# Optimization experiments

Hardware: AMD Instinct MI355X
Metric: run time of the kernel (lower is better)

The kernel has to match this reference:

```python
import jax, jax.numpy as jnp
import numpy as np

INPUT_SIZE = 128
HIDDEN_SIZE = 128
B, S = 4, 4096


def setup_inputs() -> dict:
    key = jax.random.key(0)
    ks = jax.random.split(key, 9)
    sc_in = 1.0 / np.sqrt(INPUT_SIZE)
    sc_h = 1.0 / np.sqrt(HIDDEN_SIZE)
    return {
        "x": jax.random.normal(ks[0], (B, S, INPUT_SIZE), jnp.float32),
        "Wq": jax.random.uniform(ks[1], (INPUT_SIZE, HIDDEN_SIZE), jnp.float32, -sc_in, sc_in),
        "bq": jax.random.uniform(ks[2], (HIDDEN_SIZE,), jnp.float32, -sc_in, sc_in),
        "Wk": jax.random.uniform(ks[3], (INPUT_SIZE, HIDDEN_SIZE), jnp.float32, -sc_in, sc_in),
        "bk": jax.random.uniform(ks[4], (HIDDEN_SIZE,), jnp.float32, -sc_in, sc_in),
        "Wv": jax.random.uniform(ks[5], (INPUT_SIZE, HIDDEN_SIZE), jnp.float32, -sc_in, sc_in),
        "bv": jax.random.uniform(ks[6], (HIDDEN_SIZE,), jnp.float32, -sc_in, sc_in),
        "Wo": jax.random.uniform(ks[7], (HIDDEN_SIZE, INPUT_SIZE), jnp.float32, -sc_h, sc_h),
        "bo": jax.random.uniform(ks[8], (INPUT_SIZE,), jnp.float32, -sc_h, sc_h),
    }


def reference(x, Wq, bq, Wk, bk, Wv, bv, Wo, bo):
    # single-head scaled dot-product attention (non-causal), dropout is eval-mode identity
    q = x @ Wq + bq                      # [B, S, H]
    k = x @ Wk + bk                      # [B, S, H]
    v = x @ Wv + bv                      # [B, S, H]
    scale = 1.0 / jnp.sqrt(jnp.asarray(HIDDEN_SIZE, x.dtype))
    scores = jnp.einsum("bsh,bth->bst", q, k) * scale   # [B, S, S]
    attn = jax.nn.softmax(scores, axis=-1)
    attended = jnp.einsum("bst,bth->bsh", attn, v)       # [B, S, H]
    return attended @ Wo + bo                            # [B, S, input_size]
```

## Files before the change

kernel.cpp:

```cpp
#include <hip/hip_runtime.h>
#include <stdint.h>

typedef __attribute__((ext_vector_type(8))) short short8;
typedef __attribute__((ext_vector_type(4))) float f32x4;
typedef __attribute__((ext_vector_type(16))) float f32x16;
typedef __attribute__((ext_vector_type(4))) int i32x4;
typedef __attribute__((ext_vector_type(2))) int i32x2;

#define MFMA16(a, b, c) __builtin_amdgcn_mfma_f32_16x16x32_bf16((a), (b), (c), 0, 0, 0)
#define MFMA32(a, b, c) __builtin_amdgcn_mfma_f32_32x32x16_bf16((a), (b), (c), 0, 0, 0)

typedef __attribute__((address_space(1))) const void GVoid;
typedef __attribute__((address_space(3))) void LVoid;
#define GLDS16(g, l) __builtin_amdgcn_global_load_lds((GVoid*)(g), (LVoid*)(l), 16, 0, 0)

#define L2E 1.4426950408889634f

__device__ __forceinline__ unsigned short f2bf(float f) {
  unsigned int u = __builtin_bit_cast(unsigned int, f);
  u += 0x7fffu + ((u >> 16) & 1u);
  return (unsigned short)(u >> 16);
}
__device__ __forceinline__ float bf2f(unsigned short u) {
  return __builtin_bit_cast(float, (unsigned int)u << 16);
}

__device__ __forceinline__ float fexp2(float x) {
  return __builtin_amdgcn_exp2f(x);
}

__device__ __forceinline__ i32x2 pls(int a, int b) {
  return __builtin_amdgcn_permlane32_swap(a, b, false, false);
}
__device__ __forceinline__ float fasf(int x) { return __builtin_bit_cast(float, x); }
__device__ __forceinline__ int iasi(float x) { return __builtin_bit_cast(int, x); }

__device__ __forceinline__ int cvtpk(float lo, float hi) {
  int d;
  asm("v_cvt_pk_bf16_f32 %0, %1, %2" : "=v"(d) : "v"(lo), "v"(hi));
  return d;
}

__global__ __launch_bounds__(256) void k_proj(
    const float* __restrict__ x,
    const float* __restrict__ Wq, const float* __restrict__ bq,
    const float* __restrict__ Wk, const float* __restrict__ bk,
    const float* __restrict__ Wv, const float* __restrict__ bv,
    const float* __restrict__ Wo,
    unsigned short* __restrict__ Q2, unsigned short* __restrict__ K2,
    unsigned short* __restrict__ V2, unsigned short* __restrict__ Wo2)
{
  __shared__ __align__(16) unsigned short wt[128 * 128];
  __shared__ __align__(16) unsigned short st[64 * 136];
  const int tid  = threadIdx.x;
  const int lane = tid & 63;
  const int wid  = tid >> 6;
  const int l15  = lane & 15;
  const int g    = lane >> 4;
  const int wI   = blockIdx.x >> 8;
  const int blk  = blockIdx.x & 255;
  const int r0   = blk * 64 + wid * 16;

  if (blockIdx.x == 0) {
    for (int e = tid; e < 16384; e += 256) {
      int j = e & 7, ln = (e >> 3) & 63, kt = (e >> 9) & 7, dt = e >> 12;
      int h = kt * 16 + (ln >> 5) * 8 + j, oc = dt * 32 + (ln & 31);
      Wo2[e] = f2bf(Wo[h * 128 + oc]);
    }
  }

  short8 af[4];
  {
    const float* xp = x + (r0 + l15) * 128 + g * 8;
#pragma unroll
    for (int kt = 0; kt < 4; ++kt) {
      float4 v0 = *(const float4*)(xp + kt * 32);
      float4 v1 = *(const float4*)(xp + kt * 32 + 4);
      short8 a;
      a[0] = (short)f2bf(v0.x); a[1] = (short)f2bf(v0.y);
      a[2] = (short)f2bf(v0.z); a[3] = (short)f2bf(v0.w);
      a[4] = (short)f2bf(v1.x); a[5] = (short)f2bf(v1.y);
      a[6] = (short)f2bf(v1.z); a[7] = (short)f2bf(v1.w);
      af[kt] = a;
    }
  }

  const float* W  = (wI == 0) ? Wq : (wI == 1) ? Wk : Wv;
  const float* bv_ = (wI == 0) ? bq : (wI == 1) ? bk : bv;

  for (int i = 0; i < 64; ++i) {
    int idx = i * 256 + tid;
    int k = idx >> 7, n = idx & 127;
    int cs = (k >> 3) ^ (n & 7);
    wt[n * 128 + cs * 8 + (k & 7)] = f2bf(W[idx]);
  }
  __syncthreads();

  float bias[8];
#pragma unroll
  for (int nt = 0; nt < 8; ++nt) bias[nt] = bv_[nt * 16 + l15];

  f32x4 acc[8];
#pragma unroll
  for (int nt = 0; nt < 8; ++nt) acc[nt] = (f32x4){0.f, 0.f, 0.f, 0.f};

#pragma unroll
  for (int nt = 0; nt < 8; ++nt) {
    const int n = nt * 16 + l15;
#pragma unroll
    for (int ks = 0; ks < 4; ++ks) {
      int cs = (ks * 4 + g) ^ (n & 7);
      short8 bf = *(const short8*)&wt[n * 128 + cs * 8];
      acc[nt] = MFMA16(af[ks], bf, acc[nt]);
    }
  }

  if (wI < 2) {
    const float sc = (wI == 0) ? 0.08838834764831845f : 1.0f;
#pragma unroll
    for (int nt = 0; nt < 8; ++nt) {
      int col = nt * 16 + l15;
#pragma unroll
      for (int r = 0; r < 4; ++r)
        st[(wid * 16 + g * 4 + r) * 136 + col] = f2bf((acc[nt][r] + bias[nt]) * sc);
    }
    __syncthreads();
    unsigned short* Og = (wI == 0) ? Q2 : K2;
#pragma unroll
    for (int c4 = 0; c4 < 4; ++c4) {
      int c = c4 * 256 + tid;
      int T = c >> 9, cc = c & 511;
      int kt = cc >> 6, hib = (cc >> 5) & 1, s32 = cc & 31;
      int m0 = blk * 64 + T * 32;
      int bb = m0 >> 12, tile = (m0 & 4095) >> 5;
      short8 v = *(const short8*)&st[(T * 32 + s32) * 136 + kt * 16 + hib * 8];
      *(short8*)&Og[(size_t)(bb * 128 + tile) * 4096 + cc * 8] = v;
    }
  } else {
#pragma unroll
    for (int nt = 0; nt < 8; ++nt) {
      int col = nt * 16 + l15;
      int m0 = r0 + g * 4;
      int bb = m0 >> 12, srow = m0 & 4095;
      int idx = (bb * 128 + (srow >> 5)) * 4096 + ((srow >> 4) & 1) * 2048 +
                (col >> 5) * 512 + ((srow >> 3) & 1) * 256 + (col & 31) * 8 +
                (srow & 7);
      ushort4 pk;
      pk.x = f2bf(acc[nt][0] + bias[nt]);
      pk.y = f2bf(acc[nt][1] + bias[nt]);
      pk.z = f2bf(acc[nt][2] + bias[nt]);
      pk.w = f2bf(acc[nt][3] + bias[nt]);
      *(ushort4*)&V2[idx] = pk;
    }
  }
}

__global__ __launch_bounds__(256, 2) void k_attn(
    const unsigned short* __restrict__ Q2,
    const unsigned short* __restrict__ K2,
    const unsigned short* __restrict__ V2,
    unsigned short* __restrict__ PA,
    float2* __restrict__ ML2)
{
  __shared__ __align__(16) char smem[66560];
  const int tid = threadIdx.x, lane = tid & 63, wid = tid >> 6;
  const int rr = lane & 31, hi = lane >> 5;
  const int p = blockIdx.x;
  const int b = (p & 7) >> 1;
  const int idx = ((p >> 3) << 1) | (p & 1);
  const int qst = idx >> 2, kvq = idx & 3;
  const int q0tile = qst * 4 + wid;

  short8 qf[8];
  {
    const unsigned short* qp = Q2 + (size_t)(b * 128 + q0tile) * 4096 + lane * 8;
#pragma unroll
    for (int kt = 0; kt < 8; ++kt) qf[kt] = *(const short8*)(qp + kt * 512);
  }

  const unsigned short* gsrc[4];
  gsrc[0] = K2 + (size_t)(b * 128 + kvq * 32 + 0) * 4096 + tid * 8;
  gsrc[1] = K2 + (size_t)(b * 128 + kvq * 32 + 1) * 4096 + tid * 8;
  gsrc[2] = V2 + (size_t)(b * 128 + kvq * 32 + 0) * 4096 + tid * 8;
  gsrc[3] = V2 + (size_t)(b * 128 + kvq * 32 + 1) * 4096 + tid * 8;

  char* const rbuf = smem + 65536 + wid * 128;

#pragma unroll
  for (int i = 0; i < 4; ++i) {
    GLDS16(gsrc[i], smem + i * 8192 + tid * 16);
    GLDS16(gsrc[i] + 2048, smem + i * 8192 + 4096 + tid * 16);
  }

  f32x16 O[4];
#pragma unroll
  for (int dt = 0; dt < 4; ++dt)
#pragma unroll
    for (int j = 0; j < 16; ++j) O[dt][j] = 0.f;
  f32x16 zc;
#pragma unroll
  for (int j = 0; j < 16; ++j) zc[j] = 0.f;
  float mS = -3.0e38f, lS = 0.f;

  for (int t = 0; t < 16; ++t) {
    char* const b0 = smem + (t & 1) * 32768;
    if (t < 15) {
      char* const bn = smem + ((t + 1) & 1) * 32768;
      const size_t adv = (size_t)(t + 1) * 8192;
#pragma unroll
      for (int i = 0; i < 4; ++i) {
        GLDS16(gsrc[i] + adv, bn + i * 8192 + tid * 16);
        GLDS16(gsrc[i] + adv + 2048, bn + i * 8192 + 4096 + tid * 16);
      }
      asm volatile("s_waitcnt vmcnt(8)" ::: "memory");
    } else {
      asm volatile("s_waitcnt vmcnt(0)" ::: "memory");
    }
    __builtin_amdgcn_s_barrier();
    __builtin_amdgcn_sched_barrier(0);

    f32x16 sT0, sT1;
    __builtin_amdgcn_s_setprio(1);
    {
      short8 kf[8];
#pragma unroll
      for (int kt = 0; kt < 8; ++kt)
        kf[kt] = *(const short8*)(b0 + kt * 1024 + lane * 16);
      sT0 = MFMA32(kf[0], qf[0], zc);
#pragma unroll
      for (int kt = 1; kt < 8; ++kt) sT0 = MFMA32(kf[kt], qf[kt], sT0);
    }
    {
      short8 kf[8];
#pragma unroll
      for (int kt = 0; kt < 8; ++kt)
        kf[kt] = *(const short8*)(b0 + 8192 + kt * 1024 + lane * 16);
      sT1 = MFMA32(kf[0], qf[0], zc);
#pragma unroll
      for (int kt = 1; kt < 8; ++kt) sT1 = MFMA32(kf[kt], qf[kt], sT1);
    }
    __builtin_amdgcn_s_setprio(0);

    float pm = -3.0e38f;
#pragma unroll
    for (int r = 0; r < 16; ++r) pm = fmaxf(pm, fmaxf(sT0[r], sT1[r]));
    { i32x2 r = pls(iasi(pm), iasi(pm)); pm = fmaxf(fasf(r[0]), fasf(r[1])); }

    if (!__all(pm - mS <= 8.0f)) {
      float mnew = fmaxf(mS, pm);
      float fsc = fexp2((mS - mnew) * L2E);
      mS = mnew;
      lS *= fsc;
      if (hi == 0) *(float*)(rbuf + rr * 4) = fsc;
      f32x4 fr[4];
#pragma unroll
      for (int i = 0; i < 4; ++i)
        fr[i] = *(const f32x4*)(rbuf + i * 32 + hi * 16);
#pragma unroll
      for (int dt = 0; dt < 4; ++dt)
#pragma unroll
        for (int i = 0; i < 4; ++i)
#pragma unroll
          for (int j = 0; j < 4; ++j) O[dt][i * 4 + j] *= fr[i][j];
    }

    const float mL = mS * L2E;
    float pv0[16], pv1[16];
    float ts = 0.f;
#pragma unroll
    for (int r = 0; r < 16; ++r) {
      pv0[r] = fexp2(sT0[r] * L2E - mL);
      pv1[r] = fexp2(sT1[r] * L2E - mL);
      ts += pv0[r] + pv1[r];
    }
    { i32x2 r = pls(iasi(ts), iasi(ts)); ts = fasf(r[0]) + fasf(r[1]); }
    lS += ts;

    short8 pa[4];
    {
      int dw[8];
#pragma unroll
      for (int m = 0; m < 8; ++m) dw[m] = cvtpk(pv0[2 * m], pv0[2 * m + 1]);
      i32x2 ra = pls(dw[0], dw[2]);
      i32x2 rb = pls(dw[1], dw[3]);
      i32x2 rc = pls(dw[4], dw[6]);
      i32x2 rd = pls(dw[5], dw[7]);
      i32x4 w0 = {ra[0], rb[0], ra[1], rb[1]};
      i32x4 w1 = {rc[0], rd[0], rc[1], rd[1]};
      pa[0] = __builtin_bit_cast(short8, w0);
      pa[1] = __builtin_bit_cast(short8, w1);
    }
    {
      int dw[8];
#pragma unroll
      for (int m = 0; m < 8; ++m) dw[m] = cvtpk(pv1[2 * m], pv1[2 * m + 1]);
      i32x2 ra = pls(dw[0], dw[2]);
      i32x2 rb = pls(dw[1], dw[3]);
      i32x2 rc = pls(dw[4], dw[6]);
      i32x2 rd = pls(dw[5], dw[7]);
      i32x4 w0 = {ra[0], rb[0], ra[1], rb[1]};
      i32x4 w1 = {rc[0], rd[0], rc[1], rd[1]};
      pa[2] = __builtin_bit_cast(short8, w0);
      pa[3] = __builtin_bit_cast(short8, w1);
    }

    __builtin_amdgcn_s_setprio(1);
#pragma unroll
    for (int ks = 0; ks < 4; ++ks) {
      const char* vb = b0 + 16384 + (ks >> 1) * 8192 + (ks & 1) * 4096;
      short8 vf[4];
#pragma unroll
      for (int dt = 0; dt < 4; ++dt)
        vf[dt] = *(const short8*)(vb + dt * 1024 + lane * 16);
#pragma unroll
      for (int dt = 0; dt < 4; ++dt) O[dt] = MFMA32(pa[ks], vf[dt], O[dt]);
    }
    __builtin_amdgcn_s_setprio(0);

    __builtin_amdgcn_s_barrier();
  }

  unsigned short* pab = PA + ((size_t)(b * 4 + kvq) * 128 + q0tile) * 4096;
#pragma unroll
  for (int dt = 0; dt < 4; ++dt) {
    int kt = dt * 2 + (rr >> 4);
#pragma unroll
    for (int r = 0; r < 16; ++r) {
      int q = (r & 3) + 8 * (r >> 2) + 4 * hi;
      int e = kt * 512 + (((rr >> 3) & 1) * 32 + q) * 8 + (rr & 7);
      pab[e] = f2bf(O[dt][r]);
    }
  }
  if (hi == 0)
    ML2[(size_t)(b * 4 + kvq) * 4096 + q0tile * 32 + rr] = make_float2(mS, lS);
}

__global__ __launch_bounds__(256) void k_merge(
    const unsigned short* __restrict__ PA,
    const float2* __restrict__ ML2,
    const unsigned short* __restrict__ Wo2,
    const float* __restrict__ bo,
    float* __restrict__ out)
{
  const int tid = threadIdx.x, lane = tid & 63, w = tid >> 6;
  const int rr = lane & 31, hi = lane >> 5;
  const int p = blockIdx.x;
  const int b = (p & 7) >> 1;
  const int qt32 = ((p >> 3) << 1) | (p & 1);

  float mh[4], lh[4];
#pragma unroll
  for (int h = 0; h < 4; ++h) {
    float2 ml = ML2[(size_t)(b * 4 + h) * 4096 + qt32 * 32 + rr];
    mh[h] = ml.x; lh[h] = ml.y;
  }
  float M = fmaxf(fmaxf(mh[0], mh[1]), fmaxf(mh[2], mh[3]));
  float ch[4], L = 0.f;
#pragma unroll
  for (int h = 0; h < 4; ++h) { ch[h] = fexp2((mh[h] - M) * L2E); L += ch[h] * lh[h]; }
  float iL = 1.0f / L;
#pragma unroll
  for (int h = 0; h < 4; ++h) ch[h] *= iL;

  short8 attb[8];
#pragma unroll
  for (int kt = 0; kt < 8; ++kt) {
    float a[8];
#pragma unroll
    for (int j = 0; j < 8; ++j) a[j] = 0.f;
#pragma unroll
    for (int h = 0; h < 4; ++h) {
      short8 ph = *(const short8*)(PA + ((size_t)(b * 4 + h) * 128 + qt32) * 4096 +
                                   kt * 512 + lane * 8);
#pragma unroll
      for (int j = 0; j < 8; ++j)
        a[j] += ch[h] * bf2f((unsigned short)ph[j]);
    }
    i32x4 wv = {cvtpk(a[0], a[1]), cvtpk(a[2], a[3]),
                cvtpk(a[4], a[5]), cvtpk(a[6], a[7])};
    attb[kt] = __builtin_bit_cast(short8, wv);
  }

  short8 wof[8];
#pragma unroll
  for (int kt = 0; kt < 8; ++kt)
    wof[kt] = *(const short8*)(Wo2 + (w * 8 + kt) * 512 + lane * 8);

  f32x16 zc;
#pragma unroll
  for (int j = 0; j < 16; ++j) zc[j] = 0.f;
  f32x16 acc = MFMA32(attb[0], wof[0], zc);
#pragma unroll
  for (int kt = 1; kt < 8; ++kt) acc = MFMA32(attb[kt], wof[kt], acc);

  float bov = bo[w * 32 + rr];
  float* op = out + (size_t)(b * 4096 + qt32 * 32) * 128 + w * 32 + rr;
#pragma unroll
  for (int r = 0; r < 16; ++r) {
    int q = (r & 3) + 8 * (r >> 2) + 4 * hi;
    op[q * 128] = acc[r] + bov;
  }
}

extern "C" void kernel_launch(void* const* d_in, const int* in_sizes, int n_in,
                              void* d_out, int out_size, void* d_ws, size_t ws_size,
                              hipStream_t stream) {
  const float* x  = (const float*)d_in[0];
  const float* Wq = (const float*)d_in[1];
  const float* bq = (const float*)d_in[2];
  const float* Wk = (const float*)d_in[3];
  const float* bk = (const float*)d_in[4];
  const float* Wv = (const float*)d_in[5];
  const float* bv = (const float*)d_in[6];
  const float* Wo = (const float*)d_in[7];
  const float* bo = (const float*)d_in[8];

  const size_t NE = 4u * 4096u * 128u;
  unsigned short* Q2  = (unsigned short*)d_ws;
  unsigned short* K2  = Q2 + NE;
  unsigned short* V2  = K2 + NE;
  unsigned short* Wo2 = V2 + NE;
  unsigned short* PA  = Wo2 + 16384;
  float2*         ML2 = (float2*)(PA + (size_t)16 * 128 * 4096);

  k_proj<<<768, 256, 0, stream>>>(x, Wq, bq, Wk, bk, Wv, bv, Wo, Q2, K2, V2, Wo2);
  k_attn<<<512, 256, 0, stream>>>(Q2, K2, V2, PA, ML2);
  k_merge<<<512, 256, 0, stream>>>(PA, ML2, Wo2, bo, (float*)d_out);
}
```

Measured before the change: 77.28 us.

## Halve KV tile size to fit four attention blocks per CU

Splits each 64-key KV tile into two 32-key tiles. Shared memory per block drops from about 65KB to about 33KB, and launch bounds rise from 2 to 4 blocks per CU, so more waves are resident to hide latency. The cost is twice as many loop iterations, each with its own barriers, softmax max/rescale checks and cross-lane shuffles, plus a tighter register budget that could cause spills. Tree reductions replace the serial max and sum chains.

```diff
diff --git a/kernel.cpp b/kernel.cpp
--- a/kernel.cpp
+++ b/kernel.cpp
@@ -155,14 +155,14 @@
   }
 }
 
-__global__ __launch_bounds__(256, 2) void k_attn(
+__global__ __launch_bounds__(256, 4) void k_attn(
     const unsigned short* __restrict__ Q2,
     const unsigned short* __restrict__ K2,
     const unsigned short* __restrict__ V2,
     unsigned short* __restrict__ PA,
     float2* __restrict__ ML2)
 {
-  __shared__ __align__(16) char smem[66560];
+  __shared__ __align__(16) char smem[33792];
   const int tid = threadIdx.x, lane = tid & 63, wid = tid >> 6;
   const int rr = lane & 31, hi = lane >> 5;
   const int p = blockIdx.x;
@@ -178,19 +178,15 @@
     for (int kt = 0; kt < 8; ++kt) qf[kt] = *(const short8*)(qp + kt * 512);
   }
 
-  const unsigned short* gsrc[4];
-  gsrc[0] = K2 + (size_t)(b * 128 + kvq * 32 + 0) * 4096 + tid * 8;
-  gsrc[1] = K2 + (size_t)(b * 128 + kvq * 32 + 1) * 4096 + tid * 8;
-  gsrc[2] = V2 + (size_t)(b * 128 + kvq * 32 + 0) * 4096 + tid * 8;
-  gsrc[3] = V2 + (size_t)(b * 128 + kvq * 32 + 1) * 4096 + tid * 8;
-
-  char* const rbuf = smem + 65536 + wid * 128;
-
-#pragma unroll
-  for (int i = 0; i < 4; ++i) {
-    GLDS16(gsrc[i], smem + i * 8192 + tid * 16);
-    GLDS16(gsrc[i] + 2048, smem + i * 8192 + 4096 + tid * 16);
-  }
+  const unsigned short* kbase = K2 + (size_t)(b * 128 + kvq * 32) * 4096 + tid * 8;
+  const unsigned short* vbase = V2 + (size_t)(b * 128 + kvq * 32) * 4096 + tid * 8;
+
+  char* const rbuf = smem + 32768 + wid * 128;
+
+  GLDS16(kbase,        smem + tid * 16);
+  GLDS16(kbase + 2048, smem + 4096 + tid * 16);
+  GLDS16(vbase,        smem + 8192 + tid * 16);
+  GLDS16(vbase + 2048, smem + 12288 + tid * 16);
 
   f32x16 O[4];
 #pragma unroll
@@ -202,48 +198,39 @@
   for (int j = 0; j < 16; ++j) zc[j] = 0.f;
   float mS = -3.0e38f, lS = 0.f;
 
-  for (int t = 0; t < 16; ++t) {
-    char* const b0 = smem + (t & 1) * 32768;
-    if (t < 15) {
-      char* const bn = smem + ((t + 1) & 1) * 32768;
-      const size_t adv = (size_t)(t + 1) * 8192;
-#pragma unroll
-      for (int i = 0; i < 4; ++i) {
-        GLDS16(gsrc[i] + adv, bn + i * 8192 + tid * 16);
-        GLDS16(gsrc[i] + adv + 2048, bn + i * 8192 + 4096 + tid * 16);
-      }
-      asm volatile("s_waitcnt vmcnt(8)" ::: "memory");
+  for (int t = 0; t < 32; ++t) {
+    char* const b0 = smem + (t & 1) * 16384;
+    if (t < 31) {
+      char* const bn = smem + ((t + 1) & 1) * 16384;
+      const size_t adv = (size_t)(t + 1) * 4096;
+      GLDS16(kbase + adv,        bn + tid * 16);
+      GLDS16(kbase + adv + 2048, bn + 4096 + tid * 16);
+      GLDS16(vbase + adv,        bn + 8192 + tid * 16);
+      GLDS16(vbase + adv + 2048, bn + 12288 + tid * 16);
+      asm volatile("s_waitcnt vmcnt(4)" ::: "memory");
     } else {
       asm volatile("s_waitcnt vmcnt(0)" ::: "memory");
     }
     __builtin_amdgcn_s_barrier();
     __builtin_amdgcn_sched_barrier(0);
 
-    f32x16 sT0, sT1;
+    f32x16 sT;
     __builtin_amdgcn_s_setprio(1);
     {
       short8 kf[8];
 #pragma unroll
       for (int kt = 0; kt < 8; ++kt)
         kf[kt] = *(const short8*)(b0 + kt * 1024 + lane * 16);
-      sT0 = MFMA32(kf[0], qf[0], zc);
-#pragma unroll
-      for (int kt = 1; kt < 8; ++kt) sT0 = MFMA32(kf[kt], qf[kt], sT0);
-    }
-    {
-      short8 kf[8];
-#pragma unroll
-      for (int kt = 0; kt < 8; ++kt)
-        kf[kt] = *(const short8*)(b0 + 8192 + kt * 1024 + lane * 16);
-      sT1 = MFMA32(kf[0], qf[0], zc);
-#pragma unroll
-      for (int kt = 1; kt < 8; ++kt) sT1 = MFMA32(kf[kt], qf[kt], sT1);
+      sT = MFMA32(kf[0], qf[0], zc);
+#pragma unroll
+      for (int kt = 1; kt < 8; ++kt) sT = MFMA32(kf[kt], qf[kt], sT);
     }
     __builtin_amdgcn_s_setprio(0);
 
-    float pm = -3.0e38f;
-#pragma unroll
-    for (int r = 0; r < 16; ++r) pm = fmaxf(pm, fmaxf(sT0[r], sT1[r]));
+    float pm = fmaxf(fmaxf(fmaxf(sT[0], sT[1]), fmaxf(sT[2], sT[3])),
+                     fmaxf(fmaxf(sT[4], sT[5]), fmaxf(sT[6], sT[7])));
+    pm = fmaxf(pm, fmaxf(fmaxf(fmaxf(sT[8], sT[9]), fmaxf(sT[10], sT[11])),
+                         fmaxf(fmaxf(sT[12], sT[13]), fmaxf(sT[14], sT[15]))));
     { i32x2 r = pls(iasi(pm), iasi(pm)); pm = fmaxf(fasf(r[0]), fasf(r[1])); }
 
     if (!__all(pm - mS <= 8.0f)) {
@@ -265,55 +252,46 @@
     }
 
     const float mL = mS * L2E;
-    float pv0[16], pv1[16];
-    float ts = 0.f;
-#pragma unroll
-    for (int r = 0; r < 16; ++r) {
-      pv0[r] = fexp2(sT0[r] * L2E - mL);
-      pv1[r] = fexp2(sT1[r] * L2E - mL);
-      ts += pv0[r] + pv1[r];
-    }
+    float pv[16];
+#pragma unroll
+    for (int r = 0; r < 16; ++r) pv[r] = fexp2(sT[r] * L2E - mL);
+    float s01 = (pv[0] + pv[1]) + (pv[2] + pv[3]);
+    float s23 = (pv[4] + pv[5]) + (pv[6] + pv[7]);
+    float s45 = (pv[8] + pv[9]) + (pv[10] + pv[11]);
+    float s67 = (pv[12] + pv[13]) + (pv[14] + pv[15]);
+    float ts = (s01 + s23) + (s45 + s67);
     { i32x2 r = pls(iasi(ts), iasi(ts)); ts = fasf(r[0]) + fasf(r[1]); }
     lS += ts;
 
-    short8 pa[4];
+    short8 pa0, pa1;
     {
       int dw[8];
 #pragma unroll
-      for (int m = 0; m < 8; ++m) dw[m] = cvtpk(pv0[2 * m], pv0[2 * m + 1]);
+      for (int m = 0; m < 8; ++m) dw[m] = cvtpk(pv[2 * m], pv[2 * m + 1]);
       i32x2 ra = pls(dw[0], dw[2]);
       i32x2 rb = pls(dw[1], dw[3]);
       i32x2 rc = pls(dw[4], dw[6]);
       i32x2 rd = pls(dw[5], dw[7]);
       i32x4 w0 = {ra[0], rb[0], ra[1], rb[1]};
       i32x4 w1 = {rc[0], rd[0], rc[1], rd[1]};
-      pa[0] = __builtin_bit_cast(short8, w0);
-      pa[1] = __builtin_bit_cast(short8, w1);
-    }
+      pa0 = __builtin_bit_cast(short8, w0);
+      pa1 = __builtin_bit_cast(short8, w1);
+    }
+
+    __builtin_amdgcn_s_setprio(1);
     {
-      int dw[8];
-#pragma unroll
-      for (int m = 0; m < 8; ++m) dw[m] = cvtpk(pv1[2 * m], pv1[2 * m + 1]);
-      i32x2 ra = pls(dw[0], dw[2]);
-      i32x2 rb = pls(dw[1], dw[3]);
-      i32x2 rc = pls(dw[4], dw[6]);
-      i32x2 rd = pls(dw[5], dw[7]);
-      i32x4 w0 = {ra[0], rb[0], ra[1], rb[1]};
-      i32x4 w1 = {rc[0], rd[0], rc[1], rd[1]};
-      pa[2] = __builtin_bit_cast(short8, w0);
-      pa[3] = __builtin_bit_cast(short8, w1);
-    }
-
-    __builtin_amdgcn_s_setprio(1);
-#pragma unroll
-    for (int ks = 0; ks < 4; ++ks) {
-      const char* vb = b0 + 16384 + (ks >> 1) * 8192 + (ks & 1) * 4096;
+      const char* vb = b0 + 8192;
       short8 vf[4];
 #pragma unroll
       for (int dt = 0; dt < 4; ++dt)
         vf[dt] = *(const short8*)(vb + dt * 1024 + lane * 16);
 #pragma unroll
-      for (int dt = 0; dt < 4; ++dt) O[dt] = MFMA32(pa[ks], vf[dt], O[dt]);
+      for (int dt = 0; dt < 4; ++dt) O[dt] = MFMA32(pa0, vf[dt], O[dt]);
+#pragma unroll
+      for (int dt = 0; dt < 4; ++dt)
+        vf[dt] = *(const short8*)(vb + 4096 + dt * 1024 + lane * 16);
+#pragma unroll
+      for (int dt = 0; dt < 4; ++dt) O[dt] = MFMA32(pa1, vf[dt], O[dt]);
     }
     __builtin_amdgcn_s_setprio(0);
 
```

Result: slower. 89.60 us (+15.9%).
